# Kernel optimization log

Hardware: AMD Instinct MI355X
Metric: run time of the kernel (lower is better)

The kernel has to match this reference:

```python
import jax, jax.numpy as jnp
import numpy as np

CATE_HIERARCHY = (21, 191, 1009)
CATE_EMBED_DIM = 100
B, L, D = 32, 2048, 256


def setup_inputs() -> dict:
    key = jax.random.key(0)
    ks = iter(jax.random.split(key, 32))
    inp = {"x": jax.random.normal(next(ks), (B, L, D), dtype=jnp.float32)}
    for h, C in enumerate(CATE_HIERARCHY):
        inp[f"cat_embed_{h}"] = jax.random.normal(next(ks), (C, CATE_EMBED_DIM), dtype=jnp.float32) * 0.05
        inp[f"attend_w_{h}"] = jax.random.normal(next(ks), (D, CATE_EMBED_DIM), dtype=jnp.float32) * 0.05
        inp[f"dense_w_{h}"] = jax.random.normal(next(ks), (2 * D, D), dtype=jnp.float32) * 0.05
        inp[f"dense_b_{h}"] = jnp.zeros((D,), dtype=jnp.float32)
        inp[f"pred_w_{h}"] = jax.random.normal(next(ks), (D, C), dtype=jnp.float32) * 0.05
        inp[f"pred_b_{h}"] = jnp.zeros((C,), dtype=jnp.float32)
    return inp


def _forward(x, levels):
    # x: [B, L, D]; levels: list of (cat_embed, attend_w, dense_w, dense_b, pred_w, pred_b)
    text_mean = jnp.mean(x, axis=1)  # [B, D]
    prev = None  # [B, L] recurrent category gating
    probs = []
    for ce, aw, dw, db, pw, pb in levels:
        C = ce.shape[0]
        tw = x if prev is None else x * prev[:, :, None]          # [B, L, D]
        scores = jnp.tanh(tw @ aw) @ ce.T                          # [B, L, C]
        att = jax.nn.softmax(scores, axis=1)                       # softmax over seq
        pooled = jnp.einsum('blc,bld->bd', att, tw) / C            # mean over C of batch_dot
        feat = jnp.concatenate([text_mean, pooled], axis=-1)       # [B, 2D]
        dense = jax.nn.relu(feat @ dw + db)                        # [B, D]
        pred = jax.nn.softmax(dense @ pw + pb, axis=1)             # [B, C]
        probs.append(pred)
        prev = jnp.einsum('blc,bc->bl', att, pred) / C             # mean over C
    return tuple(probs)


def reference(x,
              cat_embed_0, cat_embed_1, cat_embed_2,
              attend_w_0, attend_w_1, attend_w_2,
              dense_w_0, dense_w_1, dense_w_2,
              dense_b_0, dense_b_1, dense_b_2,
              pred_w_0, pred_w_1, pred_w_2,
              pred_b_0, pred_b_1, pred_b_2):
    levels = [
        (cat_embed_0, attend_w_0, dense_w_0, dense_b_0, pred_w_0, pred_b_0),
        (cat_embed_1, attend_w_1, dense_w_1, dense_b_1, pred_w_1, pred_b_1),
        (cat_embed_2, attend_w_2, dense_w_2, dense_b_2, pred_w_2, pred_b_2),
    ]
    return _forward(x, levels)
```

## Files before the change

kernel.cpp:

```cpp
#include <hip/hip_runtime.h>
#include <math.h>

#define LSEQ 2048
#define NB   32
#define DM   256
#define RT   65536
#define LDT  80

#define SW8(c, q) (((q) & 8) | (((q) ^ (c)) & 7))

typedef float f4 __attribute__((ext_vector_type(4)));
typedef __attribute__((ext_vector_type(4))) float f32x4;
typedef __attribute__((ext_vector_type(8))) short bf16x8;

#define MFMA16 __builtin_amdgcn_mfma_f32_16x16x32_bf16


__device__ __forceinline__ short f2bf(float f) {
  unsigned u = __float_as_uint(f);
  unsigned r = (u + 0x7fffu + ((u >> 16) & 1u)) >> 16;
  return (short)r;
}
__device__ __forceinline__ float bf2f(short s) {
  return __uint_as_float(((unsigned)(unsigned short)s) << 16);
}
__device__ __forceinline__ float tanh_fast(float z) {
  float e = __expf(2.f * z);
  return 1.f - __fdividef(2.f, 1.f + e);
}


__global__ __launch_bounds__(256) void cvt_x(const float* __restrict__ x,
                                             short* __restrict__ xh,
                                             short* __restrict__ xl) {
  long idx = ((long)blockIdx.x * 256 + threadIdx.x) * 8;
  f4 v0 = *(const f4*)(x + idx), v1 = *(const f4*)(x + idx + 4);
  float vv[8] = {v0[0], v0[1], v0[2], v0[3], v1[0], v1[1], v1[2], v1[3]};
  bf16x8 h, l;
#pragma unroll
  for (int i = 0; i < 8; ++i) {
    short hh = f2bf(vv[i]);
    h[i] = hh;
    l[i] = f2bf(vv[i] - bf2f(hh));
  }
  *(bf16x8*)(xh + idx) = h;
  *(bf16x8*)(xl + idx) = l;
}


__global__ __launch_bounds__(256) void tm_partial_k(const float* __restrict__ x,
                                                    float* __restrict__ tp) {
  int lc = blockIdx.x, b = blockIdx.y, d = threadIdx.x;
  const float* xp = x + ((long)b * LSEQ + lc * 128) * DM + d;
  float a = 0.f;
#pragma unroll 8
  for (int i = 0; i < 128; ++i) a += xp[(long)i * DM];
  tp[((long)lc * NB + b) * DM + d] = a;
}

__global__ __launch_bounds__(256) void tm_reduce_k(const float* __restrict__ tp,
                                                   float* __restrict__ tm) {
  int idx = blockIdx.x * 256 + threadIdx.x;
  int b = idx >> 8, d = idx & 255;
  float a = 0.f;
#pragma unroll
  for (int lc = 0; lc < 16; ++lc) a += tp[((long)lc * NB + b) * DM + d];
  tm[idx] = a * (1.f / LSEQ);
}


__global__ __launch_bounds__(256) void cvt_ce(const float* __restrict__ ce,
                                              short* __restrict__ h,
                                              short* __restrict__ l, int C) {
  int idx = blockIdx.x * 256 + threadIdx.x;
  int c = idx >> 7, k = idx & 127;
  float v = (c < C && k < 100) ? ce[c * 100 + k] : 0.f;
  short hh = f2bf(v);
  h[idx] = hh;
  l[idx] = f2bf(v - bf2f(hh));
}

__global__ __launch_bounds__(256) void cvt_aw(const float* __restrict__ aw,
                                              short* __restrict__ h,
                                              short* __restrict__ l) {
  int idx = blockIdx.x * 256 + threadIdx.x;
  int e = idx >> 8, k = idx & 255;
  float v = (e < 100) ? aw[k * 100 + e] : 0.f;
  short hh = f2bf(v);
  h[idx] = hh;
  l[idx] = f2bf(v - bf2f(hh));
}


__global__ __launch_bounds__(256) void s_mfma(const short* __restrict__ xh,
                                              const short* __restrict__ xl,
                                              const short* __restrict__ awh,
                                              const short* __restrict__ awl,
                                              const float* __restrict__ prevb,
                                              short* __restrict__ sGh,
                                              short* __restrict__ sGl, int hasPrev) {
  __shared__ __align__(16) short bufh[8192];
  __shared__ __align__(16) short bufl[8192];
  const int tid = threadIdx.x, lane = tid & 63, wv = tid >> 6;
  const int lo = lane & 15, hi = lane >> 4;
  const int st = blockIdx.y;
  const long r0 = (long)blockIdx.x * 128 + wv * 32;

  float pv[2][4];
#pragma unroll
  for (int m = 0; m < 2; ++m)
#pragma unroll
    for (int q = 0; q < 4; ++q)
      pv[m][q] = hasPrev ? prevb[r0 + m * 16 + hi * 4 + q] : 1.f;

  f32x4 acc[2][4];
#pragma unroll
  for (int m = 0; m < 2; ++m)
#pragma unroll
    for (int n = 0; n < 4; ++n) acc[m][n] = (f32x4){0.f, 0.f, 0.f, 0.f};

#pragma unroll 1
  for (int kh = 0; kh < 2; ++kh) {
    __syncthreads();
    {
      const short* gh = awh + (long)st * 64 * 256 + kh * 128;
      const short* gl = awl + (long)st * 64 * 256 + kh * 128;
#pragma unroll
      for (int j = 0; j < 4; ++j) {
        int slot = tid + j * 256;
        int c = slot >> 4, q = slot & 15;
        int dst = c * 128 + SW8(c, q) * 8;
        *(bf16x8*)(bufh + dst) = *(const bf16x8*)(gh + (long)c * 256 + q * 8);
        *(bf16x8*)(bufl + dst) = *(const bf16x8*)(gl + (long)c * 256 + q * 8);
      }
    }
    bf16x8 Ah[2][4], Al[2][4];
#pragma unroll
    for (int m = 0; m < 2; ++m)
#pragma unroll
      for (int ks = 0; ks < 4; ++ks) {
        long off = (r0 + m * 16 + lo) * 256 + kh * 128 + ks * 32 + hi * 8;
        Ah[m][ks] = *(const bf16x8*)(xh + off);
        Al[m][ks] = *(const bf16x8*)(xl + off);
      }
    __syncthreads();
#pragma unroll
    for (int ks = 0; ks < 4; ++ks) {
      bf16x8 Bh[4], Bl[4];
#pragma unroll
      for (int n = 0; n < 4; ++n) {
        int c = n * 16 + lo;
        int idx = c * 128 + SW8(c, ks * 4 + hi) * 8;
        Bh[n] = *(const bf16x8*)(bufh + idx);
        Bl[n] = *(const bf16x8*)(bufl + idx);
      }
#pragma unroll
      for (int n = 0; n < 4; ++n) {
        acc[0][n] = MFMA16(Ah[0][ks], Bh[n], acc[0][n], 0, 0, 0);
        acc[1][n] = MFMA16(Ah[1][ks], Bh[n], acc[1][n], 0, 0, 0);
        acc[0][n] = MFMA16(Al[0][ks], Bh[n], acc[0][n], 0, 0, 0);
        acc[1][n] = MFMA16(Al[1][ks], Bh[n], acc[1][n], 0, 0, 0);
        acc[0][n] = MFMA16(Ah[0][ks], Bl[n], acc[0][n], 0, 0, 0);
        acc[1][n] = MFMA16(Ah[1][ks], Bl[n], acc[1][n], 0, 0, 0);
      }
    }
  }

#pragma unroll
  for (int m = 0; m < 2; ++m)
#pragma unroll
    for (int n = 0; n < 4; ++n)
#pragma unroll
      for (int q = 0; q < 4; ++q) {
        long r = r0 + m * 16 + hi * 4 + q;
        int c = st * 64 + n * 16 + lo;
        float t = tanh_fast(pv[m][q] * acc[m][n][q]);
        short hh = f2bf(t);
        sGh[r * 128 + c] = hh;
        sGl[r * 128 + c] = f2bf(t - bf2f(hh));
      }
}


__device__ __forceinline__ void load_afrags(const short* __restrict__ sGh,
                                            const short* __restrict__ sGl,
                                            long r0, int lo, int hi,
                                            bf16x8 (&Ah)[2][4], bf16x8 (&Al)[2][4]) {
#pragma unroll
  for (int m = 0; m < 2; ++m)
#pragma unroll
    for (int ks = 0; ks < 4; ++ks) {
      long off = (r0 + m * 16 + lo) * 128 + ks * 32 + hi * 8;
      Ah[m][ks] = *(const bf16x8*)(sGh + off);
      Al[m][ks] = *(const bf16x8*)(sGl + off);
    }
}


__global__ __launch_bounds__(256) void mfma_colP(const short* __restrict__ sGh,
                                                 const short* __restrict__ sGl,
                                                 const short* __restrict__ ceh,
                                                 const short* __restrict__ cel,
                                                 float* __restrict__ partial,
                                                 short* __restrict__ P,
                                                 int cpb, int CP) {
  __shared__ __align__(16) short bufh[8192];
  __shared__ __align__(16) short bufl[8192];
  __shared__ __align__(16) short tlds[4][32 * LDT];
  const int tid = threadIdx.x, lane = tid & 63, wv = tid >> 6;
  const int lo = lane & 15, hi = lane >> 4;
  const long r0 = (long)blockIdx.x * 128 + wv * 32;
  const long gw = (long)blockIdx.x * 4 + wv;
  const int s0 = blockIdx.y * cpb;
  const int oct = lane & 7;

  bf16x8 Ah[2][4], Al[2][4];
  load_afrags(sGh, sGl, r0, lo, hi, Ah, Al);

#pragma unroll 1
  for (int s = 0; s < cpb; ++s) {
    const int c0s = (s0 + s) * 64;
    __syncthreads();
    {
      const short* gh = ceh + (long)c0s * 128;
      const short* gl = cel + (long)c0s * 128;
#pragma unroll
      for (int j = 0; j < 4; ++j) {
        int slot = tid + j * 256;
        int c = slot >> 4, q = slot & 15;
        int dst = c * 128 + SW8(c, q) * 8;
        *(bf16x8*)(bufh + dst) = *(const bf16x8*)(gh + slot * 8);
        *(bf16x8*)(bufl + dst) = *(const bf16x8*)(gl + slot * 8);
      }
    }
    __syncthreads();

    f32x4 acc[2][4];
#pragma unroll
    for (int m = 0; m < 2; ++m)
#pragma unroll
      for (int n = 0; n < 4; ++n) acc[m][n] = (f32x4){0.f, 0.f, 0.f, 0.f};

#pragma unroll
    for (int ks = 0; ks < 4; ++ks) {
      bf16x8 Bh[4], Bl[4];
#pragma unroll
      for (int n = 0; n < 4; ++n) {
        int c = n * 16 + lo;
        int idx = c * 128 + SW8(c, ks * 4 + hi) * 8;
        Bh[n] = *(const bf16x8*)(bufh + idx);
        Bl[n] = *(const bf16x8*)(bufl + idx);
      }
#pragma unroll
      for (int n = 0; n < 4; ++n) {
        acc[0][n] = MFMA16(Ah[0][ks], Bh[n], acc[0][n], 0, 0, 0);
        acc[1][n] = MFMA16(Ah[1][ks], Bh[n], acc[1][n], 0, 0, 0);
        acc[0][n] = MFMA16(Al[0][ks], Bh[n], acc[0][n], 0, 0, 0);
        acc[1][n] = MFMA16(Al[1][ks], Bh[n], acc[1][n], 0, 0, 0);
        acc[0][n] = MFMA16(Ah[0][ks], Bl[n], acc[0][n], 0, 0, 0);
        acc[1][n] = MFMA16(Ah[1][ks], Bl[n], acc[1][n], 0, 0, 0);
      }
    }

#pragma unroll
    for (int n = 0; n < 4; ++n) {
      float sum = 0.f;
#pragma unroll
      for (int m = 0; m < 2; ++m)
#pragma unroll
        for (int q = 0; q < 4; ++q) {
          float e = __expf(acc[m][n][q]);
          sum += e;
          tlds[wv][(m * 16 + hi * 4 + q) * LDT + n * 16 + lo] = f2bf(e);
        }
      sum += __shfl_xor(sum, 16);
      sum += __shfl_xor(sum, 32);
      if (lane < 16) partial[gw * 1024 + c0s + n * 16 + lane] = sum;
    }
#pragma unroll
    for (int j = 0; j < 4; ++j) {
      int rl = (lane >> 3) + j * 8;
      bf16x8 v = *(const bf16x8*)(&tlds[wv][rl * LDT + oct * 8]);
      *(bf16x8*)(P + (r0 + rl) * (long)CP + c0s + oct * 8) = v;
    }
  }
}


__global__ __launch_bounds__(256) void wz_kernel(const float* __restrict__ partial,
                                                 float* __restrict__ Z,
                                                 float* __restrict__ w, int C) {
  int idx = blockIdx.x * 256 + threadIdx.x;
  int b = idx >> 10, c = idx & 1023;
  float z = 0.f;
#pragma unroll 8
  for (int i = 0; i < 64; ++i) z += partial[(long)(b * 64 + i) * 1024 + c];
  Z[idx] = z;
  w[idx] = (c < C) ? 1.f / ((float)C * z) : 0.f;
}


__global__ __launch_bounds__(256) void rowpass_k(const short* __restrict__ P,
                                                 const float* __restrict__ w,
                                                 const float* __restrict__ ps,
                                                 float* __restrict__ out, int CP) {
  const int lane = threadIdx.x & 63, wv = threadIdx.x >> 6;
  const long r = (long)blockIdx.x * 4 + wv;
  const int b = (int)(r >> 11);
  const short* Pr = P + r * (long)CP;
  const float* wb_ = w + b * 1024;
  float acc = 0.f;
  for (int c0 = lane * 8; c0 < CP; c0 += 512) {
    bf16x8 pv = *(const bf16x8*)(Pr + c0);
    f4 w0 = *(const f4*)(wb_ + c0);
    f4 w1 = *(const f4*)(wb_ + c0 + 4);
    acc = fmaf(bf2f(pv[0]), w0[0], acc);
    acc = fmaf(bf2f(pv[1]), w0[1], acc);
    acc = fmaf(bf2f(pv[2]), w0[2], acc);
    acc = fmaf(bf2f(pv[3]), w0[3], acc);
    acc = fmaf(bf2f(pv[4]), w1[0], acc);
    acc = fmaf(bf2f(pv[5]), w1[1], acc);
    acc = fmaf(bf2f(pv[6]), w1[2], acc);
    acc = fmaf(bf2f(pv[7]), w1[3], acc);
  }
  acc += __shfl_xor(acc, 1);
  acc += __shfl_xor(acc, 2);
  acc += __shfl_xor(acc, 4);
  acc += __shfl_xor(acc, 8);
  acc += __shfl_xor(acc, 16);
  acc += __shfl_xor(acc, 32);
  if (lane == 0) out[r] = ps ? acc * ps[r] : acc;
}


__global__ __launch_bounds__(256) void pooled_partial_k(const short* __restrict__ xh,
                                                        const float* __restrict__ gs,
                                                        float* __restrict__ pp) {
  int lc = blockIdx.x, b = blockIdx.y;
  int rr = threadIdx.x >> 7, dd = threadIdx.x & 127;
  long rbase = (long)b * LSEQ + lc * 256 + rr * 128;
  const short* xp = xh + rbase * DM + dd * 2;
  const float* gp = gs + rbase;
  float a0 = 0.f, a1 = 0.f;
#pragma unroll 4
  for (int i = 0; i < 128; ++i) {
    unsigned v = *(const unsigned*)(xp + (long)i * DM);
    float g = gp[i];
    a0 = fmaf(g, __uint_as_float((v & 0xffffu) << 16), a0);
    a1 = fmaf(g, __uint_as_float(v & 0xffff0000u), a1);
  }
  float* dst = pp + ((long)(lc * 2 + rr) * NB + b) * DM + dd * 2;
  dst[0] = a0;
  dst[1] = a1;
}

__global__ __launch_bounds__(256) void pooled_reduce_k(const float* __restrict__ pp,
                                                       float* __restrict__ pooled) {
  int idx = blockIdx.x * 256 + threadIdx.x;
  int b = idx >> 8, d = idx & 255;
  float a = 0.f;
#pragma unroll
  for (int lc = 0; lc < 16; ++lc) a += pp[((long)lc * NB + b) * DM + d];
  pooled[idx] = a;
}


__global__ __launch_bounds__(256) void dense_k(const float* __restrict__ tm,
                                               const float* __restrict__ pooled,
                                               const float* __restrict__ dw,
                                               const float* __restrict__ db,
                                               float* __restrict__ dense) {
  __shared__ float f[2 * DM];
  int b = blockIdx.x, t = threadIdx.x;
  f[t] = tm[b * DM + t];
  f[DM + t] = pooled[b * DM + t];
  __syncthreads();
  float a = db[t];
#pragma unroll 8
  for (int k = 0; k < 2 * DM; ++k) a = fmaf(f[k], dw[(long)k * DM + t], a);
  dense[b * DM + t] = fmaxf(a, 0.f);
}


__global__ __launch_bounds__(256) void logits_k(const float* __restrict__ dense,
                                                const float* __restrict__ pw,
                                                const float* __restrict__ pb,
                                                float* __restrict__ logits, int C) {
  __shared__ float dS[DM];
  int b = blockIdx.y, t = threadIdx.x;
  int c = blockIdx.x * 256 + t;
  dS[t] = dense[b * DM + t];
  __syncthreads();
  if (c < C) {
    float a = pb[c];
#pragma unroll 8
    for (int k = 0; k < DM; ++k) a = fmaf(dS[k], pw[(long)k * C + c], a);
    logits[b * 1024 + c] = a;
  }
}


__global__ __launch_bounds__(256) void softmax_k(const float* __restrict__ logits,
                                                 const float* __restrict__ Z,
                                                 float* __restrict__ out,
                                                 float* __restrict__ w,
                                                 int C, int writeW) {
  __shared__ float buf[1024];
  __shared__ float red[256];
  int b = blockIdx.x, t = threadIdx.x;
  float m = -1e30f;
  for (int c = t; c < C; c += 256) {
    float v = logits[b * 1024 + c];
    buf[c] = v;
    m = fmaxf(m, v);
  }
  red[t] = m;
  __syncthreads();
  for (int s2 = 128; s2 > 0; s2 >>= 1) {
    if (t < s2) red[t] = fmaxf(red[t], red[t + s2]);
    __syncthreads();
  }
  m = red[0];
  __syncthreads();
  float sum = 0.f;
  for (int c = t; c < C; c += 256) {
    float e = __expf(buf[c] - m);
    buf[c] = e;
    sum += e;
  }
  red[t] = sum;
  __syncthreads();
  for (int s2 = 128; s2 > 0; s2 >>= 1) {
    if (t < s2) red[t] += red[t + s2];
    __syncthreads();
  }
  float inv = 1.f / red[0];
  for (int c = t; c < C; c += 256) out[(long)b * C + c] = buf[c] * inv;
  if (writeW) {
    float invC = 1.f / (float)C;
    for (int c = t; c < 1024; c += 256)
      w[b * 1024 + c] = (c < C) ? (buf[c] * inv) * invC / Z[b * 1024 + c] : 0.f;
  }
}


extern "C" void kernel_launch(void* const* d_in, const int* in_sizes, int n_in,
                              void* d_out, int out_size, void* d_ws, size_t ws_size,
                              hipStream_t stream) {
  (void)in_sizes; (void)n_in; (void)out_size; (void)ws_size;
  const float* x = (const float*)d_in[0];

  const int Cs[3]     = {21, 191, 1009};
  const int CPs[3]    = {64, 192, 1024};
  const int SGs[3]    = {1, 3, 4};
  const int CPBs[3]   = {1, 1, 4};
  const int outoff[3] = {0, 672, 6784};

  char* base = (char*)d_ws;
  short* xh  = (short*)base; base += (size_t)RT * 256 * 2;
  short* xl  = (short*)base; base += (size_t)RT * 256 * 2;
  short* sGh = (short*)base; base += (size_t)RT * 128 * 2;
  short* sGl = (short*)base; base += (size_t)RT * 128 * 2;
  short* Pb  = (short*)base; base += (size_t)RT * 1024 * 2;
  short* ceh = (short*)base; base += (size_t)3 * 131072 * 2;
  short* cel = (short*)base; base += (size_t)3 * 131072 * 2;
  short* awh = (short*)base; base += (size_t)3 * 32768 * 2;
  short* awl = (short*)base; base += (size_t)3 * 32768 * 2;
  float* partial = (float*)base; base += (size_t)2048 * 1024 * 4;
  float* Zb     = (float*)base; base += 32768 * 4;
  float* wb     = (float*)base; base += 32768 * 4;
  float* gs     = (float*)base; base += RT * 4;
  float* prevb  = (float*)base; base += RT * 4;
  float* tp     = (float*)base; base += 131072 * 4;
  float* tm     = (float*)base; base += 8192 * 4;
  float* pp     = (float*)base; base += 131072 * 4;
  float* pooled = (float*)base; base += 8192 * 4;
  float* dense  = (float*)base; base += 8192 * 4;
  float* logits = (float*)base; base += 32768 * 4;

  cvt_x<<<8192, 256, 0, stream>>>(x, xh, xl);
  tm_partial_k<<<dim3(16, NB), 256, 0, stream>>>(x, tp);
  tm_reduce_k<<<32, 256, 0, stream>>>(tp, tm);
  for (int h = 0; h < 3; ++h) {
    cvt_ce<<<512, 256, 0, stream>>>((const float*)d_in[1 + 6 * h], ceh + h * 131072,
                                    cel + h * 131072, Cs[h]);
    cvt_aw<<<128, 256, 0, stream>>>((const float*)d_in[1 + 6 * h + 1], awh + h * 32768,
                                    awl + h * 32768);
  }

  for (int h = 0; h < 3; ++h) {
    const float* dw = (const float*)d_in[1 + 6 * h + 2];
    const float* db = (const float*)d_in[1 + 6 * h + 3];
    const float* pw = (const float*)d_in[1 + 6 * h + 4];
    const float* pb = (const float*)d_in[1 + 6 * h + 5];
    const short* ch = ceh + h * 131072;
    const short* cl = cel + h * 131072;
    const int C = Cs[h], CP = CPs[h], SG = SGs[h], CPB = CPBs[h];

    s_mfma<<<dim3(512, 2), 256, 0, stream>>>(xh, xl, awh + h * 32768, awl + h * 32768,
                                             prevb, sGh, sGl, h > 0 ? 1 : 0);
    mfma_colP<<<dim3(512, SG), 256, 0, stream>>>(sGh, sGl, ch, cl, partial, Pb, CPB, CP);
    wz_kernel<<<128, 256, 0, stream>>>(partial, Zb, wb, C);
    rowpass_k<<<RT / 4, 256, 0, stream>>>(Pb, wb, h > 0 ? prevb : nullptr, gs, CP);
    pooled_partial_k<<<dim3(8, NB), 256, 0, stream>>>(xh, gs, pp);
    pooled_reduce_k<<<32, 256, 0, stream>>>(pp, pooled);
    dense_k<<<NB, 256, 0, stream>>>(tm, pooled, dw, db, dense);
    logits_k<<<dim3((C + 255) / 256, NB), 256, 0, stream>>>(dense, pw, pb, logits, C);
    softmax_k<<<NB, 256, 0, stream>>>(logits, Zb, (float*)d_out + outoff[h], wb, C,
                                      h < 2 ? 1 : 0);
    if (h < 2)
      rowpass_k<<<RT / 4, 256, 0, stream>>>(Pb, wb, nullptr, prevb, CP);
  }
}
```

Measured before the change: 529.4 us.

## Fuse x conversion with text-mean, reuse A fragments across column tiles

Merges the bf16 hi/lo split of x into the text-mean partial-sum kernel, so x is read from global memory once instead of twice. s_mfma now loops over both 64-column output tiles inside one block, loading the x fragments once rather than once per blockIdx.y. mfma_colP reuses the staging LDS for its per-wave transpose buffer and processes more column tiles per block, with fewer blocks along y. The trade-off is less grid parallelism and larger per-thread register state, and the fused conversion kernel writes its bf16 stores as 2-byte column-strided accesses.

```diff
diff --git a/kernel.cpp b/kernel.cpp
--- a/kernel.cpp
+++ b/kernel.cpp
@@ -30,31 +30,24 @@
 }
 
 
-__global__ __launch_bounds__(256) void cvt_x(const float* __restrict__ x,
-                                             short* __restrict__ xh,
-                                             short* __restrict__ xl) {
-  long idx = ((long)blockIdx.x * 256 + threadIdx.x) * 8;
-  f4 v0 = *(const f4*)(x + idx), v1 = *(const f4*)(x + idx + 4);
-  float vv[8] = {v0[0], v0[1], v0[2], v0[3], v1[0], v1[1], v1[2], v1[3]};
-  bf16x8 h, l;
-#pragma unroll
-  for (int i = 0; i < 8; ++i) {
-    short hh = f2bf(vv[i]);
-    h[i] = hh;
-    l[i] = f2bf(vv[i] - bf2f(hh));
-  }
-  *(bf16x8*)(xh + idx) = h;
-  *(bf16x8*)(xl + idx) = l;
-}
-
-
-__global__ __launch_bounds__(256) void tm_partial_k(const float* __restrict__ x,
-                                                    float* __restrict__ tp) {
+__global__ __launch_bounds__(256) void cvt_x_tm(const float* __restrict__ x,
+                                                short* __restrict__ xh,
+                                                short* __restrict__ xl,
+                                                float* __restrict__ tp) {
   int lc = blockIdx.x, b = blockIdx.y, d = threadIdx.x;
-  const float* xp = x + ((long)b * LSEQ + lc * 128) * DM + d;
+  long rbase = (long)b * LSEQ + lc * 128;
+  const float* xp = x + rbase * DM + d;
+  short* xhp = xh + rbase * DM + d;
+  short* xlp = xl + rbase * DM + d;
   float a = 0.f;
-#pragma unroll 8
-  for (int i = 0; i < 128; ++i) a += xp[(long)i * DM];
+#pragma unroll 4
+  for (int i = 0; i < 128; ++i) {
+    float v = xp[(long)i * DM];
+    a += v;
+    short hh = f2bf(v);
+    xhp[(long)i * DM] = hh;
+    xlp[(long)i * DM] = f2bf(v - bf2f(hh));
+  }
   tp[((long)lc * NB + b) * DM + d] = a;
 }
 
@@ -99,11 +92,11 @@
                                               const float* __restrict__ prevb,
                                               short* __restrict__ sGh,
                                               short* __restrict__ sGl, int hasPrev) {
-  __shared__ __align__(16) short bufh[8192];
-  __shared__ __align__(16) short bufl[8192];
+  __shared__ __align__(16) short smem[16384];
+  short* bufh = smem;
+  short* bufl = smem + 8192;
   const int tid = threadIdx.x, lane = tid & 63, wv = tid >> 6;
   const int lo = lane & 15, hi = lane >> 4;
-  const int st = blockIdx.y;
   const long r0 = (long)blockIdx.x * 128 + wv * 32;
 
   float pv[2][4];
@@ -113,27 +106,16 @@
     for (int q = 0; q < 4; ++q)
       pv[m][q] = hasPrev ? prevb[r0 + m * 16 + hi * 4 + q] : 1.f;
 
-  f32x4 acc[2][4];
-#pragma unroll
-  for (int m = 0; m < 2; ++m)
-#pragma unroll
-    for (int n = 0; n < 4; ++n) acc[m][n] = (f32x4){0.f, 0.f, 0.f, 0.f};
+  f32x4 acc[2][2][4];
+#pragma unroll
+  for (int st = 0; st < 2; ++st)
+#pragma unroll
+    for (int m = 0; m < 2; ++m)
+#pragma unroll
+      for (int n = 0; n < 4; ++n) acc[st][m][n] = (f32x4){0.f, 0.f, 0.f, 0.f};
 
 #pragma unroll 1
   for (int kh = 0; kh < 2; ++kh) {
-    __syncthreads();
-    {
-      const short* gh = awh + (long)st * 64 * 256 + kh * 128;
-      const short* gl = awl + (long)st * 64 * 256 + kh * 128;
-#pragma unroll
-      for (int j = 0; j < 4; ++j) {
-        int slot = tid + j * 256;
-        int c = slot >> 4, q = slot & 15;
-        int dst = c * 128 + SW8(c, q) * 8;
-        *(bf16x8*)(bufh + dst) = *(const bf16x8*)(gh + (long)c * 256 + q * 8);
-        *(bf16x8*)(bufl + dst) = *(const bf16x8*)(gl + (long)c * 256 + q * 8);
-      }
-    }
     bf16x8 Ah[2][4], Al[2][4];
 #pragma unroll
     for (int m = 0; m < 2; ++m)
@@ -143,7 +125,123 @@
         Ah[m][ks] = *(const bf16x8*)(xh + off);
         Al[m][ks] = *(const bf16x8*)(xl + off);
       }
+#pragma unroll 1
+    for (int st = 0; st < 2; ++st) {
+      __syncthreads();
+      {
+        const short* gh = awh + (long)st * 64 * 256 + kh * 128;
+        const short* gl = awl + (long)st * 64 * 256 + kh * 128;
+#pragma unroll
+        for (int j = 0; j < 4; ++j) {
+          int slot = tid + j * 256;
+          int c = slot >> 4, q = slot & 15;
+          int dst = c * 128 + SW8(c, q) * 8;
+          *(bf16x8*)(bufh + dst) = *(const bf16x8*)(gh + (long)c * 256 + q * 8);
+          *(bf16x8*)(bufl + dst) = *(const bf16x8*)(gl + (long)c * 256 + q * 8);
+        }
+      }
+      __syncthreads();
+#pragma unroll
+      for (int ks = 0; ks < 4; ++ks) {
+        bf16x8 Bh[4], Bl[4];
+#pragma unroll
+        for (int n = 0; n < 4; ++n) {
+          int c = n * 16 + lo;
+          int idx = c * 128 + SW8(c, ks * 4 + hi) * 8;
+          Bh[n] = *(const bf16x8*)(bufh + idx);
+          Bl[n] = *(const bf16x8*)(bufl + idx);
+        }
+#pragma unroll
+        for (int n = 0; n < 4; ++n) {
+          acc[st][0][n] = MFMA16(Ah[0][ks], Bh[n], acc[st][0][n], 0, 0, 0);
+          acc[st][1][n] = MFMA16(Ah[1][ks], Bh[n], acc[st][1][n], 0, 0, 0);
+          acc[st][0][n] = MFMA16(Al[0][ks], Bh[n], acc[st][0][n], 0, 0, 0);
+          acc[st][1][n] = MFMA16(Al[1][ks], Bh[n], acc[st][1][n], 0, 0, 0);
+          acc[st][0][n] = MFMA16(Ah[0][ks], Bl[n], acc[st][0][n], 0, 0, 0);
+          acc[st][1][n] = MFMA16(Ah[1][ks], Bl[n], acc[st][1][n], 0, 0, 0);
+        }
+      }
+    }
+  }
+
+#pragma unroll
+  for (int st = 0; st < 2; ++st)
+#pragma unroll
+    for (int m = 0; m < 2; ++m)
+#pragma unroll
+      for (int n = 0; n < 4; ++n)
+#pragma unroll
+        for (int q = 0; q < 4; ++q) {
+          long r = r0 + m * 16 + hi * 4 + q;
+          int c = st * 64 + n * 16 + lo;
+          float t = tanh_fast(pv[m][q] * acc[st][m][n][q]);
+          short hh = f2bf(t);
+          sGh[r * 128 + c] = hh;
+          sGl[r * 128 + c] = f2bf(t - bf2f(hh));
+        }
+}
+
+
+__device__ __forceinline__ void load_afrags(const short* __restrict__ sGh,
+                                            const short* __restrict__ sGl,
+                                            long r0, int lo, int hi,
+                                            bf16x8 (&Ah)[2][4], bf16x8 (&Al)[2][4]) {
+#pragma unroll
+  for (int m = 0; m < 2; ++m)
+#pragma unroll
+    for (int ks = 0; ks < 4; ++ks) {
+      long off = (r0 + m * 16 + lo) * 128 + ks * 32 + hi * 8;
+      Ah[m][ks] = *(const bf16x8*)(sGh + off);
+      Al[m][ks] = *(const bf16x8*)(sGl + off);
+    }
+}
+
+
+__global__ __launch_bounds__(256) void mfma_colP(const short* __restrict__ sGh,
+                                                 const short* __restrict__ sGl,
+                                                 const short* __restrict__ ceh,
+                                                 const short* __restrict__ cel,
+                                                 float* __restrict__ partial,
+                                                 short* __restrict__ P,
+                                                 int cpb, int CP) {
+  __shared__ __align__(16) short smem[16384];
+  short* bufh = smem;
+  short* bufl = smem + 8192;
+  const int tid = threadIdx.x, lane = tid & 63, wv = tid >> 6;
+  const int lo = lane & 15, hi = lane >> 4;
+  const long r0 = (long)blockIdx.x * 128 + wv * 32;
+  const long gw = (long)blockIdx.x * 4 + wv;
+  const int s0 = blockIdx.y * cpb;
+  const int oct = lane & 7;
+  short* tw = smem + wv * (32 * LDT);
+
+  bf16x8 Ah[2][4], Al[2][4];
+  load_afrags(sGh, sGl, r0, lo, hi, Ah, Al);
+
+#pragma unroll 1
+  for (int s = 0; s < cpb; ++s) {
+    const int c0s = (s0 + s) * 64;
     __syncthreads();
+    {
+      const short* gh = ceh + (long)c0s * 128;
+      const short* gl = cel + (long)c0s * 128;
+#pragma unroll
+      for (int j = 0; j < 4; ++j) {
+        int slot = tid + j * 256;
+        int c = slot >> 4, q = slot & 15;
+        int dst = c * 128 + SW8(c, q) * 8;
+        *(bf16x8*)(bufh + dst) = *(const bf16x8*)(gh + slot * 8);
+        *(bf16x8*)(bufl + dst) = *(const bf16x8*)(gl + slot * 8);
+      }
+    }
+    __syncthreads();
+
+    f32x4 acc[2][4];
+#pragma unroll
+    for (int m = 0; m < 2; ++m)
+#pragma unroll
+      for (int n = 0; n < 4; ++n) acc[m][n] = (f32x4){0.f, 0.f, 0.f, 0.f};
+
 #pragma unroll
     for (int ks = 0; ks < 4; ++ks) {
       bf16x8 Bh[4], Bl[4];
@@ -164,103 +262,7 @@
         acc[1][n] = MFMA16(Ah[1][ks], Bl[n], acc[1][n], 0, 0, 0);
       }
     }
-  }
-
-#pragma unroll
-  for (int m = 0; m < 2; ++m)
-#pragma unroll
-    for (int n = 0; n < 4; ++n)
-#pragma unroll
-      for (int q = 0; q < 4; ++q) {
-        long r = r0 + m * 16 + hi * 4 + q;
-        int c = st * 64 + n * 16 + lo;
-        float t = tanh_fast(pv[m][q] * acc[m][n][q]);
-        short hh = f2bf(t);
-        sGh[r * 128 + c] = hh;
-        sGl[r * 128 + c] = f2bf(t - bf2f(hh));
-      }
-}
-
-
-__device__ __forceinline__ void load_afrags(const short* __restrict__ sGh,
-                                            const short* __restrict__ sGl,
-                                            long r0, int lo, int hi,
-                                            bf16x8 (&Ah)[2][4], bf16x8 (&Al)[2][4]) {
-#pragma unroll
-  for (int m = 0; m < 2; ++m)
-#pragma unroll
-    for (int ks = 0; ks < 4; ++ks) {
-      long off = (r0 + m * 16 + lo) * 128 + ks * 32 + hi * 8;
-      Ah[m][ks] = *(const bf16x8*)(sGh + off);
-      Al[m][ks] = *(const bf16x8*)(sGl + off);
-    }
-}
-
-
-__global__ __launch_bounds__(256) void mfma_colP(const short* __restrict__ sGh,
-                                                 const short* __restrict__ sGl,
-                                                 const short* __restrict__ ceh,
-                                                 const short* __restrict__ cel,
-                                                 float* __restrict__ partial,
-                                                 short* __restrict__ P,
-                                                 int cpb, int CP) {
-  __shared__ __align__(16) short bufh[8192];
-  __shared__ __align__(16) short bufl[8192];
-  __shared__ __align__(16) short tlds[4][32 * LDT];
-  const int tid = threadIdx.x, lane = tid & 63, wv = tid >> 6;
-  const int lo = lane & 15, hi = lane >> 4;
-  const long r0 = (long)blockIdx.x * 128 + wv * 32;
-  const long gw = (long)blockIdx.x * 4 + wv;
-  const int s0 = blockIdx.y * cpb;
-  const int oct = lane & 7;
-
-  bf16x8 Ah[2][4], Al[2][4];
-  load_afrags(sGh, sGl, r0, lo, hi, Ah, Al);
-
-#pragma unroll 1
-  for (int s = 0; s < cpb; ++s) {
-    const int c0s = (s0 + s) * 64;
     __syncthreads();
-    {
-      const short* gh = ceh + (long)c0s * 128;
-      const short* gl = cel + (long)c0s * 128;
-#pragma unroll
-      for (int j = 0; j < 4; ++j) {
-        int slot = tid + j * 256;
-        int c = slot >> 4, q = slot & 15;
-        int dst = c * 128 + SW8(c, q) * 8;
-        *(bf16x8*)(bufh + dst) = *(const bf16x8*)(gh + slot * 8);
-        *(bf16x8*)(bufl + dst) = *(const bf16x8*)(gl + slot * 8);
-      }
-    }
-    __syncthreads();
-
-    f32x4 acc[2][4];
-#pragma unroll
-    for (int m = 0; m < 2; ++m)
-#pragma unroll
-      for (int n = 0; n < 4; ++n) acc[m][n] = (f32x4){0.f, 0.f, 0.f, 0.f};
-
-#pragma unroll
-    for (int ks = 0; ks < 4; ++ks) {
-      bf16x8 Bh[4], Bl[4];
-#pragma unroll
-      for (int n = 0; n < 4; ++n) {
-        int c = n * 16 + lo;
-        int idx = c * 128 + SW8(c, ks * 4 + hi) * 8;
-        Bh[n] = *(const bf16x8*)(bufh + idx);
-        Bl[n] = *(const bf16x8*)(bufl + idx);
-      }
-#pragma unroll
-      for (int n = 0; n < 4; ++n) {
-        acc[0][n] = MFMA16(Ah[0][ks], Bh[n], acc[0][n], 0, 0, 0);
-        acc[1][n] = MFMA16(Ah[1][ks], Bh[n], acc[1][n], 0, 0, 0);
-        acc[0][n] = MFMA16(Al[0][ks], Bh[n], acc[0][n], 0, 0, 0);
-        acc[1][n] = MFMA16(Al[1][ks], Bh[n], acc[1][n], 0, 0, 0);
-        acc[0][n] = MFMA16(Ah[0][ks], Bl[n], acc[0][n], 0, 0, 0);
-        acc[1][n] = MFMA16(Ah[1][ks], Bl[n], acc[1][n], 0, 0, 0);
-      }
-    }
 
 #pragma unroll
     for (int n = 0; n < 4; ++n) {
@@ -271,7 +273,7 @@
         for (int q = 0; q < 4; ++q) {
           float e = __expf(acc[m][n][q]);
           sum += e;
-          tlds[wv][(m * 16 + hi * 4 + q) * LDT + n * 16 + lo] = f2bf(e);
+          tw[(m * 16 + hi * 4 + q) * LDT + n * 16 + lo] = f2bf(e);
         }
       sum += __shfl_xor(sum, 16);
       sum += __shfl_xor(sum, 32);
@@ -280,7 +282,7 @@
 #pragma unroll
     for (int j = 0; j < 4; ++j) {
       int rl = (lane >> 3) + j * 8;
-      bf16x8 v = *(const bf16x8*)(&tlds[wv][rl * LDT + oct * 8]);
+      bf16x8 v = *(const bf16x8*)(&tw[rl * LDT + oct * 8]);
       *(bf16x8*)(P + (r0 + rl) * (long)CP + c0s + oct * 8) = v;
     }
   }
@@ -452,8 +454,8 @@
 
   const int Cs[3]     = {21, 191, 1009};
   const int CPs[3]    = {64, 192, 1024};
-  const int SGs[3]    = {1, 3, 4};
-  const int CPBs[3]   = {1, 1, 4};
+  const int SGs[3]    = {1, 1, 2};
+  const int CPBs[3]   = {1, 3, 8};
   const int outoff[3] = {0, 672, 6784};
 
   char* base = (char*)d_ws;
@@ -478,8 +480,7 @@
   float* dense  = (float*)base; base += 8192 * 4;
   float* logits = (float*)base; base += 32768 * 4;
 
-  cvt_x<<<8192, 256, 0, stream>>>(x, xh, xl);
-  tm_partial_k<<<dim3(16, NB), 256, 0, stream>>>(x, tp);
+  cvt_x_tm<<<dim3(16, NB), 256, 0, stream>>>(x, xh, xl, tp);
   tm_reduce_k<<<32, 256, 0, stream>>>(tp, tm);
   for (int h = 0; h < 3; ++h) {
     cvt_ce<<<512, 256, 0, stream>>>((const float*)d_in[1 + 6 * h], ceh + h * 131072,
@@ -497,8 +498,8 @@
     const short* cl = cel + h * 131072;
     const int C = Cs[h], CP = CPs[h], SG = SGs[h], CPB = CPBs[h];
 
-    s_mfma<<<dim3(512, 2), 256, 0, stream>>>(xh, xl, awh + h * 32768, awl + h * 32768,
-                                             prevb, sGh, sGl, h > 0 ? 1 : 0);
+    s_mfma<<<512, 256, 0, stream>>>(xh, xl, awh + h * 32768, awl + h * 32768,
+                                    prevb, sGh, sGl, h > 0 ? 1 : 0);
     mfma_colP<<<dim3(512, SG), 256, 0, stream>>>(sGh, sGl, ch, cl, partial, Pb, CPB, CP);
     wz_kernel<<<128, 256, 0, stream>>>(partial, Zb, wb, C);
     rowpass_k<<<RT / 4, 256, 0, stream>>>(Pb, wb, h > 0 ? prevb : nullptr, gs, CP);
```

New measurement: 628.0 us. 18.6% more time.
